# Kernel tuning notes

Hardware: AMD Instinct MI355X
Metric: run time of the kernel (lower is better)

Reference implementation:

```python
import jax, jax.numpy as jnp
import numpy as np

H = 12       # heads
D = 768      # hidden size
DH = D // H  # head dim = 64
SCALE = 1.0 / jnp.sqrt(jnp.float32(DH))
LN_EPS = 1e-3  # keras LayerNormalization default epsilon


def setup_inputs() -> dict:
    key = jax.random.key(0)
    ks = jax.random.split(key, 8)
    B, L = 16, 512
    s = 0.02  # truncated-normal-ish init scale
    return {
        "x": jax.random.normal(ks[0], (B, L, D), jnp.float32),
        "mask": jnp.ones((B, L), jnp.int32),
        "Wq": jax.random.normal(ks[1], (D, D), jnp.float32) * s,
        "bq": jnp.zeros((D,), jnp.float32),
        "Wk": jax.random.normal(ks[2], (D, D), jnp.float32) * s,
        "bk": jnp.zeros((D,), jnp.float32),
        "Wv": jax.random.normal(ks[3], (D, D), jnp.float32) * s,
        "bv": jnp.zeros((D,), jnp.float32),
        "Wo": jax.random.normal(ks[4], (D, D), jnp.float32) * s,
        "bo": jnp.zeros((D,), jnp.float32),
        "gamma": jnp.ones((D,), jnp.float32),
        "beta": jnp.zeros((D,), jnp.float32),
    }


def reference(x, mask, Wq, bq, Wk, bk, Wv, bv, Wo, bo, gamma, beta):
    B, L, _ = x.shape
    # QKV projections, split into heads: [B, L, H, DH]
    q = (x @ Wq + bq).reshape(B, L, H, DH)
    k = (x @ Wk + bk).reshape(B, L, H, DH)
    v = (x @ Wv + bv).reshape(B, L, H, DH)
    # scaled dot-product scores: [B, H, Lq, Lk]
    scores = jnp.einsum('bqhd,bkhd->bhqk', q, k) * SCALE
    # key-side padding mask (mask==0 -> -inf)
    neg = jnp.float32(-1e9)
    scores = jnp.where(mask[:, None, None, :] > 0, scores, neg)
    p = jax.nn.softmax(scores, axis=-1)
    # dropout rate fixed to 0.0 -> identity
    ctx = jnp.einsum('bhqk,bkhd->bqhd', p, v).reshape(B, L, D)
    attn_out = ctx @ Wo + bo
    # residual + LayerNorm (keras default eps=1e-3)
    y = x + attn_out
    mu = jnp.mean(y, axis=-1, keepdims=True)
    var = jnp.mean(jnp.square(y - mu), axis=-1, keepdims=True)
    return gamma * (y - mu) * jax.lax.rsqrt(var + LN_EPS) + beta
```

## Files before the change

kernel.cpp:

```cpp
#include <hip/hip_runtime.h>
#include <math.h>

#define NH 12
#define DMODEL 768
#define DHEAD 64
#define BATCH 16
#define SEQ 512
#define NTOK (BATCH*SEQ)
#define ATTN_SCALE 0.125f
#define LN_EPS 1e-3f
#define PADP 72
#define NKT 12

typedef __attribute__((ext_vector_type(8))) short  bf16x8;
typedef __attribute__((ext_vector_type(4))) float  f32x4;

__device__ __forceinline__ unsigned short f2bf(float f) {
    unsigned int u = __float_as_uint(f);
    unsigned int r = (u + 0x7fffu + ((u >> 16) & 1u)) >> 16;
    return (unsigned short)r;
}

__device__ __forceinline__ void async_copy16(const void* g, void* l) {
    __builtin_amdgcn_global_load_lds((const __attribute__((address_space(1))) void*)g,
                                     (__attribute__((address_space(3))) void*)l,
                                     16, 0, 0);
}

#define SBAR() do { \
    __builtin_amdgcn_sched_barrier(0); \
    __builtin_amdgcn_s_barrier(); \
    __builtin_amdgcn_sched_barrier(0); \
} while (0)

#define VMW0() do { \
    __builtin_amdgcn_sched_barrier(0); \
    asm volatile("s_waitcnt vmcnt(0)" ::: "memory"); \
    __builtin_amdgcn_sched_barrier(0); \
} while (0)

__global__ __launch_bounds__(256) void prep_kernel(
    const float* __restrict__ x,
    const float* __restrict__ Wq, const float* __restrict__ Wk,
    const float* __restrict__ Wv, const float* __restrict__ Wo,
    unsigned short* __restrict__ xb,
    unsigned short* __restrict__ tq, unsigned short* __restrict__ tk,
    unsigned short* __restrict__ tv, unsigned short* __restrict__ to_)
{
    __shared__ float tile[32][33];
    const int bid = blockIdx.x;
    const int tid = threadIdx.x;

    if (bid < 6144) {
        int i = (bid * 256 + tid) * 4;
        const float4 v = *(const float4*)(x + i);
        unsigned long long pack =
              (unsigned long long)f2bf(v.x)
            | ((unsigned long long)f2bf(v.y) << 16)
            | ((unsigned long long)f2bf(v.z) << 32)
            | ((unsigned long long)f2bf(v.w) << 48);
        *(unsigned long long*)(xb + i) = pack;
        return;
    }

    const int t   = bid - 6144;
    const int zz  = t / 576;
    const int rem = t % 576;
    const float* W = (zz == 0) ? Wq : (zz == 1) ? Wk : (zz == 2) ? Wv : Wo;
    unsigned short* T = (zz == 0) ? tq : (zz == 1) ? tk : (zz == 2) ? tv : to_;

    const int bx = (rem / 24) * 32;
    const int by = (rem % 24) * 32;
    const int tx = tid & 31, ty = tid >> 5;

    #pragma unroll
    for (int i = 0; i < 32; i += 8)
        tile[ty + i][tx] = W[(size_t)(bx + ty + i) * DMODEL + by + tx];
    __syncthreads();
    #pragma unroll
    for (int i = 0; i < 32; i += 8)
        T[(size_t)(by + ty + i) * DMODEL + bx + tx] = f2bf(tile[tx][ty + i]);
}

#define QSTAGE(kt, sb) do { \
    const int _k0 = (kt) * 64; \
    _Pragma("unroll") \
    for (int _i = 0; _i < 4; ++_i) \
        async_copy16(aSrc + (size_t)_i * (8 * DMODEL) + _k0, &As[sb][(w * 4 + _i) * 512]); \
    _Pragma("unroll") \
    for (int _i = 0; _i < 4; ++_i) \
        async_copy16(bSrc + (size_t)_i * (64 * DMODEL) + _k0, &Bs[sb][(w + 8 * _i) * 512]); \
    if (w < 4) \
        async_copy16(bSrc + (size_t)4 * (64 * DMODEL) + _k0, &Bs[sb][(w + 32) * 512]); \
} while (0)

#define QTILE(t, c, o, hasNext) do { \
    if (hasNext) QSTAGE((t) + 1, o); \
    bf16x8 aF[4][2]; \
    _Pragma("unroll") \
    for (int _m = 0; _m < 4; ++_m) { \
        const int _row = wm * 64 + _m * 16 + l16; \
        aF[_m][0] = *(const bf16x8*)&As[c][_row * 64 + p0]; \
        aF[_m][1] = *(const bf16x8*)&As[c][_row * 64 + (p0 ^ 32)]; \
    } \
    _Pragma("unroll") \
    for (int _nh = 0; _nh < 3; ++_nh) { \
        bf16x8 bF[3][2]; \
        _Pragma("unroll") \
        for (int _n = 0; _n < 3; ++_n) { \
            const int _row = wn * 144 + (_nh * 3 + _n) * 16 + l16; \
            bF[_n][0] = *(const bf16x8*)&Bs[c][_row * 64 + p0]; \
            bF[_n][1] = *(const bf16x8*)&Bs[c][_row * 64 + (p0 ^ 32)]; \
        } \
        __builtin_amdgcn_s_setprio(1); \
        _Pragma("unroll") \
        for (int _k = 0; _k < 2; ++_k) \
          _Pragma("unroll") \
          for (int _m = 0; _m < 4; ++_m) \
            _Pragma("unroll") \
            for (int _n = 0; _n < 3; ++_n) \
              acc[_m][_nh * 3 + _n] = __builtin_amdgcn_mfma_f32_16x16x32_bf16( \
                  aF[_m][_k], bF[_n][_k], acc[_m][_nh * 3 + _n], 0, 0, 0); \
        __builtin_amdgcn_s_setprio(0); \
    } \
    if (hasNext) VMW0(); \
    SBAR(); \
} while (0)

__global__ __launch_bounds__(512, 2) void gemm_db_qkv(
    const unsigned short* __restrict__ xb, const unsigned short* __restrict__ wt,
    const float* __restrict__ bq, const float* __restrict__ bk, const float* __restrict__ bv,
    unsigned short* __restrict__ o0, unsigned short* __restrict__ o1,
    unsigned short* __restrict__ o2)
{
    __shared__ __align__(16) unsigned short As[2][256 * 64];
    __shared__ __align__(16) unsigned short Bs[2][288 * 64];

    const int orig = blockIdx.x;
    const int wg   = (orig & 7) * 32 + (orig >> 3);
    const int m0   = (wg >> 3) * 256;
    const int n0   = (wg & 7) * 288;

    const int tid  = threadIdx.x;
    const int lane = tid & 63;
    const int w    = tid >> 6;
    const int wm   = w >> 1, wn = w & 1;
    const int quad = lane >> 4;
    const int l16  = lane & 15;
    const int rloc = lane >> 3;
    const int csw  = (lane & 7) ^ rloc;
    const int p0   = (quad ^ (l16 & 7)) * 8;

    const unsigned short* aSrc = xb + (size_t)(m0 + w * 32 + rloc) * DMODEL + csw * 8;
    const unsigned short* bSrc = wt + (size_t)(n0 + w * 8  + rloc) * DMODEL + csw * 8;

    f32x4 acc[4][9] = {};

    QSTAGE(0, 0);
    VMW0();
    SBAR();

    #pragma unroll 1
    for (int tt = 0; tt < NKT / 2; ++tt) {
        QTILE(2 * tt,     0, 1, 1);
        QTILE(2 * tt + 1, 1, 0, (tt < NKT / 2 - 1));
    }

    #pragma unroll
    for (int nf = 0; nf < 9; ++nf) {
        const int ncg = n0 + wn * 144 + nf * 16 + l16;
        const int zz  = (ncg >= 1536) ? 2 : (ncg >= 768) ? 1 : 0;
        const int ncl = ncg - zz * 768;
        const int h = ncl >> 6, dh = ncl & 63;
        const float bval = ((zz == 0) ? bq : (zz == 1) ? bk : bv)[ncl];
        if (zz == 2) {
            #pragma unroll
            for (int mi = 0; mi < 4; ++mi) {
                const int mbase = m0 + wm * 64 + mi * 16 + quad * 4;
                const int bi = mbase >> 9, l = mbase & 511;
                unsigned long long pack = 0;
                #pragma unroll
                for (int r = 0; r < 4; ++r)
                    pack |= (unsigned long long)f2bf(acc[mi][nf][r] + bval) << (16 * r);
                *(unsigned long long*)(o2 + ((size_t)((bi * NH + h) * DHEAD + dh)) * SEQ + l) = pack;
            }
        } else {
            const float sc = (zz == 0) ? ATTN_SCALE : 1.0f;
            unsigned short* out = (zz == 0) ? o0 : o1;
            #pragma unroll
            for (int mi = 0; mi < 4; ++mi) {
                const int mbase = m0 + wm * 64 + mi * 16 + quad * 4;
                #pragma unroll
                for (int r = 0; r < 4; ++r) {
                    const int t = mbase + r;
                    const int bi = t >> 9, l = t & 511;
                    out[(size_t)((bi * NH + h) * SEQ + l) * DHEAD + dh] =
                        f2bf((acc[mi][nf][r] + bval) * sc);
                }
            }
        }
    }
}

#define OSTAGE(kt, sb) do { \
    const int _k0 = (kt) * 64; \
    _Pragma("unroll") \
    for (int _i = 0; _i < 2; ++_i) \
        async_copy16(aSrc + (size_t)_i * (8 * DMODEL) + _k0, &Ao[sb][(w * 2 + _i) * 512]); \
    _Pragma("unroll") \
    for (int _i = 0; _i < 3; ++_i) \
        async_copy16(bSrc + (size_t)_i * (8 * DMODEL) + _k0, &Bo[sb][(w * 3 + _i) * 512]); \
} while (0)

#define OTILE(t, c, o, hasNext) do { \
    if (hasNext) OSTAGE((t) + 1, o); \
    bf16x8 aF[4][2], bF[3][2]; \
    _Pragma("unroll") \
    for (int _m = 0; _m < 4; ++_m) { \
        const int _row = wm * 64 + _m * 16 + l16; \
        aF[_m][0] = *(const bf16x8*)&Ao[c][_row * 64 + p0]; \
        aF[_m][1] = *(const bf16x8*)&Ao[c][_row * 64 + (p0 ^ 32)]; \
    } \
    _Pragma("unroll") \
    for (int _n = 0; _n < 3; ++_n) { \
        const int _row = wn * 48 + _n * 16 + l16; \
        bF[_n][0] = *(const bf16x8*)&Bo[c][_row * 64 + p0]; \
        bF[_n][1] = *(const bf16x8*)&Bo[c][_row * 64 + (p0 ^ 32)]; \
    } \
    __builtin_amdgcn_s_setprio(1); \
    _Pragma("unroll") \
    for (int _k = 0; _k < 2; ++_k) \
      _Pragma("unroll") \
      for (int _m = 0; _m < 4; ++_m) \
        _Pragma("unroll") \
        for (int _n = 0; _n < 3; ++_n) \
          acc[_m][_n] = __builtin_amdgcn_mfma_f32_16x16x32_bf16( \
              aF[_m][_k], bF[_n][_k], acc[_m][_n], 0, 0, 0); \
    __builtin_amdgcn_s_setprio(0); \
    if (hasNext) VMW0(); \
    SBAR(); \
} while (0)

__global__ __launch_bounds__(512, 2) void gemm_db_oproj(
    const unsigned short* __restrict__ ctxb, const unsigned short* __restrict__ wto,
    const float* __restrict__ bo, const float* __restrict__ x,
    float* __restrict__ y)
{
    __shared__ __align__(16) unsigned short Ao[2][132 * 64];
    __shared__ __align__(16) unsigned short Bo[2][192 * 64];

    const int orig = blockIdx.x;
    const int wg   = (orig & 7) * 32 + (orig >> 3);
    const int m0   = (wg >> 2) * 128;
    const int n0   = (wg & 3) * 192;

    const int tid  = threadIdx.x;
    const int lane = tid & 63;
    const int w    = tid >> 6;
    const int wm   = w >> 2, wn = w & 3;
    const int quad = lane >> 4;
    const int l16  = lane & 15;
    const int rloc = lane >> 3;
    const int csw  = (lane & 7) ^ rloc;
    const int p0   = (quad ^ (l16 & 7)) * 8;

    const unsigned short* aSrc = ctxb + (size_t)(m0 + w * 16 + rloc) * DMODEL + csw * 8;
    const unsigned short* bSrc = wto  + (size_t)(n0 + w * 24 + rloc) * DMODEL + csw * 8;

    f32x4 acc[4][3] = {};

    OSTAGE(0, 0);
    VMW0();
    SBAR();

    #pragma unroll 1
    for (int tt = 0; tt < NKT / 2; ++tt) {
        OTILE(2 * tt,     0, 1, 1);
        OTILE(2 * tt + 1, 1, 0, (tt < NKT / 2 - 1));
    }

    #pragma unroll
    for (int ni = 0; ni < 3; ++ni) {
        const int ncol = n0 + wn * 48 + ni * 16 + l16;
        const float bv_ = bo[ncol];
        #pragma unroll
        for (int mi = 0; mi < 4; ++mi) {
            const int mbase = m0 + wm * 64 + mi * 16 + quad * 4;
            #pragma unroll
            for (int r = 0; r < 4; ++r) {
                const size_t idx = (size_t)(mbase + r) * DMODEL + ncol;
                y[idx] = acc[mi][ni][r] + bv_ + x[idx];
            }
        }
    }
}

__global__ __launch_bounds__(256) void attn_mfma_kernel(
    const unsigned short* __restrict__ q, const unsigned short* __restrict__ k,
    const unsigned short* __restrict__ vt, const int* __restrict__ mask,
    unsigned short* __restrict__ ctxb)
{
    __shared__ __align__(16) unsigned short Qs[64 * 64];
    __shared__ __align__(16) unsigned short Ks[2][64 * 64];
    __shared__ __align__(16) unsigned short Vs[2][64 * 64];
    __shared__ __align__(16) unsigned short Ps[64 * PADP];
    __shared__ float maskV[SEQ];
    __shared__ int   cleanS[8];

    const int tid  = threadIdx.x;
    const int lane = tid & 63;
    const int w    = tid >> 6;
    const int quad = lane >> 4;
    const int l16  = lane & 15;

    const int id = blockIdx.x;
    const int qt = id / (BATCH * NH);
    const int g  = id % (BATCH * NH);
    const int b  = g / NH, h = g % NH;
    const int q0 = qt * 64;

    const unsigned short* qp  = q  + ((size_t)(b * NH + h) * SEQ + q0) * DHEAD;
    const unsigned short* kp  = k  + (size_t)(b * NH + h) * SEQ * DHEAD;
    const unsigned short* vtp = vt + (size_t)(b * NH + h) * DHEAD * SEQ;

    const int rloc = lane >> 3;
    const int csw  = (lane & 7) ^ rloc;
    const int p0   = (quad ^ (l16 & 7)) * 8;

    #pragma unroll
    for (int ii = 0; ii < 2; ++ii) {
        const int inst = 2 * w + ii;
        async_copy16(qp  + (size_t)(inst * 8 + rloc) * DHEAD + csw * 8, Qs + inst * 512);
        async_copy16(kp  + (size_t)(inst * 8 + rloc) * DHEAD + csw * 8, &Ks[0][inst * 512]);
        async_copy16(vtp + (size_t)(inst * 8 + rloc) * SEQ + csw * 8,   &Vs[0][inst * 512]);
    }
    #pragma unroll
    for (int j = 0; j < 2; ++j) {
        const int idx = tid + 256 * j;
        const bool pm = mask[b * SEQ + idx] > 0;
        maskV[idx] = pm ? 0.f : -1e9f;
        const unsigned long long bb = __ballot(pm);
        if (lane == 0) cleanS[w + 4 * j] = (bb == ~0ull) ? 1 : 0;
    }
    __syncthreads();

    bf16x8 aQ[2];
    #pragma unroll
    for (int ks = 0; ks < 2; ++ks)
        aQ[ks] = *(const bf16x8*)&Qs[(w * 16 + l16) * 64 + (p0 ^ (ks * 32))];

    bf16x8 ones;
    #pragma unroll
    for (int j = 0; j < 8; ++j) ones[j] = (short)0x3F80;

    f32x4 o[4] = {};
    f32x4 lsum = {0.f, 0.f, 0.f, 0.f};
    const f32x4 zf = {0.f, 0.f, 0.f, 0.f};

    #pragma unroll
    for (int it = 0; it < 8; ++it) {
        const int cur = it & 1;
        if (it + 1 < 8) {
            const int kt1 = (it + 1) * 64;
            #pragma unroll
            for (int ii = 0; ii < 2; ++ii) {
                const int inst = 2 * w + ii;
                async_copy16(kp  + (size_t)(kt1 + inst * 8 + rloc) * DHEAD + csw * 8,
                             &Ks[1 - cur][inst * 512]);
                async_copy16(vtp + (size_t)(inst * 8 + rloc) * SEQ + kt1 + csw * 8,
                             &Vs[1 - cur][inst * 512]);
            }
        }
        const int kt = it * 64;

        f32x4 s[4];
        #pragma unroll
        for (int ni = 0; ni < 4; ++ni) {
            bf16x8 bK0 = *(const bf16x8*)&Ks[cur][(ni * 16 + l16) * 64 + p0];
            bf16x8 bK1 = *(const bf16x8*)&Ks[cur][(ni * 16 + l16) * 64 + (p0 ^ 32)];
            f32x4 t0 = __builtin_amdgcn_mfma_f32_16x16x32_bf16(aQ[0], bK0, zf, 0, 0, 0);
            s[ni] = __builtin_amdgcn_mfma_f32_16x16x32_bf16(aQ[1], bK1, t0, 0, 0, 0);
        }
        if (cleanS[it] == 0) {
            #pragma unroll
            for (int ni = 0; ni < 4; ++ni) {
                const float mk = maskV[kt + ni * 16 + l16];
                #pragma unroll
                for (int r = 0; r < 4; ++r) s[ni][r] += mk;
            }
        }

        #pragma unroll
        for (int ni = 0; ni < 4; ++ni)
            #pragma unroll
            for (int r = 0; r < 4; ++r)
                Ps[(w * 16 + quad * 4 + r) * PADP + ni * 16 + l16]
                    = (unsigned short)(__float_as_uint(__expf(s[ni][r])) >> 16);

        bf16x8 aP[2];
        #pragma unroll
        for (int ks = 0; ks < 2; ++ks)
            aP[ks] = *(const bf16x8*)&Ps[(w * 16 + l16) * PADP + quad * 8 + ks * 32];

        lsum = __builtin_amdgcn_mfma_f32_16x16x32_bf16(aP[0], ones, lsum, 0, 0, 0);
        lsum = __builtin_amdgcn_mfma_f32_16x16x32_bf16(aP[1], ones, lsum, 0, 0, 0);

        #pragma unroll
        for (int ni = 0; ni < 4; ++ni) {
            bf16x8 bV0 = *(const bf16x8*)&Vs[cur][(ni * 16 + l16) * 64 + p0];
            bf16x8 bV1 = *(const bf16x8*)&Vs[cur][(ni * 16 + l16) * 64 + (p0 ^ 32)];
            o[ni] = __builtin_amdgcn_mfma_f32_16x16x32_bf16(aP[0], bV0, o[ni], 0, 0, 0);
            o[ni] = __builtin_amdgcn_mfma_f32_16x16x32_bf16(aP[1], bV1, o[ni], 0, 0, 0);
        }

        __syncthreads();
    }

    #pragma unroll
    for (int r = 0; r < 4; ++r) {
        const float inv = 1.f / lsum[r];
        const int tok = q0 + w * 16 + quad * 4 + r;
        #pragma unroll
        for (int ni = 0; ni < 4; ++ni)
            ctxb[(size_t)(b * SEQ + tok) * DMODEL + h * DHEAD + ni * 16 + l16]
                = f2bf(o[ni][r] * inv);
    }
}

__global__ __launch_bounds__(256) void ln_kernel(
    const float* __restrict__ y, const float* __restrict__ gamma,
    const float* __restrict__ beta, float* __restrict__ out)
{
    const int t   = blockIdx.x;
    const int tid = threadIdx.x;
    const float* row = y + (size_t)t * DMODEL;

    float vals[3];
    float s = 0.f, s2 = 0.f;
    #pragma unroll
    for (int i = 0; i < 3; ++i) {
        float vv = row[tid + 256 * i];
        vals[i] = vv;
        s  += vv;
        s2 += vv * vv;
    }
    #pragma unroll
    for (int off = 32; off > 0; off >>= 1) {
        s  += __shfl_down(s,  off);
        s2 += __shfl_down(s2, off);
    }
    __shared__ float rbuf[8];
    int w = tid >> 6;
    if ((tid & 63) == 0) { rbuf[w] = s; rbuf[4 + w] = s2; }
    __syncthreads();
    float ts  = rbuf[0] + rbuf[1] + rbuf[2] + rbuf[3];
    float ts2 = rbuf[4] + rbuf[5] + rbuf[6] + rbuf[7];
    float mu  = ts * (1.f / DMODEL);
    float var = ts2 * (1.f / DMODEL) - mu * mu;
    float inv = rsqrtf(var + LN_EPS);
    #pragma unroll
    for (int i = 0; i < 3; ++i) {
        int c = tid + 256 * i;
        out[(size_t)t * DMODEL + c] = gamma[c] * (vals[i] - mu) * inv + beta[c];
    }
}

extern "C" void kernel_launch(void* const* d_in, const int* in_sizes, int n_in,
                              void* d_out, int out_size, void* d_ws, size_t ws_size,
                              hipStream_t stream) {
    const float* x     = (const float*)d_in[0];
    const int*   mask  = (const int*)  d_in[1];
    const float* Wq    = (const float*)d_in[2];
    const float* bq    = (const float*)d_in[3];
    const float* Wk    = (const float*)d_in[4];
    const float* bk    = (const float*)d_in[5];
    const float* Wv    = (const float*)d_in[6];
    const float* bv    = (const float*)d_in[7];
    const float* Wo    = (const float*)d_in[8];
    const float* bo    = (const float*)d_in[9];
    const float* gamma = (const float*)d_in[10];
    const float* beta  = (const float*)d_in[11];
    float* out = (float*)d_out;

    const size_t perTok = (size_t)NTOK * DMODEL;
    const size_t perW   = (size_t)DMODEL * DMODEL;

    unsigned short* xb   = (unsigned short*)d_ws;
    unsigned short* wtq  = xb + perTok;
    unsigned short* wtk  = wtq + perW;
    unsigned short* wtv  = wtk + perW;
    unsigned short* wto  = wtv + perW;
    unsigned short* qb   = wto + perW;
    unsigned short* kb   = qb + perTok;
    unsigned short* vb   = kb + perTok;
    unsigned short* ctxb = vb + perTok;
    float* y = out;

    prep_kernel<<<6144 + 2304, 256, 0, stream>>>(
        x, Wq, Wk, Wv, Wo, xb, wtq, wtk, wtv, wto);

    gemm_db_qkv<<<256, 512, 0, stream>>>(xb, wtq, bq, bk, bv, qb, kb, vb);

    attn_mfma_kernel<<<dim3((SEQ / 64) * BATCH * NH), 256, 0, stream>>>(
        qb, kb, vb, mask, ctxb);

    gemm_db_oproj<<<256, 512, 0, stream>>>(ctxb, wto, bo, x, y);

    ln_kernel<<<NTOK, 256, 0, stream>>>(y, gamma, beta, out);
}
```

Baseline: 194.4 us.

## Process two query tiles per attention block to reuse K/V tiles

Each attention block now handles 128 query rows (two 64-row tiles) instead of 64, so each K/V tile loaded into shared memory feeds twice as many MFMAs and the grid is halved. Q fragments are loaded straight from global memory into registers rather than staged through LDS. The mask is now always added, with the exp folded in, replacing the per-tile clean-mask check. A launch-bounds occupancy hint is added. This roughly doubles accumulator registers and halves the number of blocks (768), which may reduce latency hiding and lowers the block count relative to the CU count.

```diff
diff --git a/kernel.cpp b/kernel.cpp
--- a/kernel.cpp
+++ b/kernel.cpp
@@ -295,17 +295,15 @@
     }
 }
 
-__global__ __launch_bounds__(256) void attn_mfma_kernel(
+__global__ __launch_bounds__(256, 3) void attn_mfma_kernel(
     const unsigned short* __restrict__ q, const unsigned short* __restrict__ k,
     const unsigned short* __restrict__ vt, const int* __restrict__ mask,
     unsigned short* __restrict__ ctxb)
 {
-    __shared__ __align__(16) unsigned short Qs[64 * 64];
     __shared__ __align__(16) unsigned short Ks[2][64 * 64];
     __shared__ __align__(16) unsigned short Vs[2][64 * 64];
-    __shared__ __align__(16) unsigned short Ps[64 * PADP];
+    __shared__ __align__(16) unsigned short Ps[2][64 * PADP];
     __shared__ float maskV[SEQ];
-    __shared__ int   cleanS[8];
 
     const int tid  = threadIdx.x;
     const int lane = tid & 63;
@@ -317,7 +315,7 @@
     const int qt = id / (BATCH * NH);
     const int g  = id % (BATCH * NH);
     const int b  = g / NH, h = g % NH;
-    const int q0 = qt * 64;
+    const int q0 = qt * 128;
 
     const unsigned short* qp  = q  + ((size_t)(b * NH + h) * SEQ + q0) * DHEAD;
     const unsigned short* kp  = k  + (size_t)(b * NH + h) * SEQ * DHEAD;
@@ -330,32 +328,32 @@
     #pragma unroll
     for (int ii = 0; ii < 2; ++ii) {
         const int inst = 2 * w + ii;
-        async_copy16(qp  + (size_t)(inst * 8 + rloc) * DHEAD + csw * 8, Qs + inst * 512);
         async_copy16(kp  + (size_t)(inst * 8 + rloc) * DHEAD + csw * 8, &Ks[0][inst * 512]);
         async_copy16(vtp + (size_t)(inst * 8 + rloc) * SEQ + csw * 8,   &Vs[0][inst * 512]);
     }
     #pragma unroll
     for (int j = 0; j < 2; ++j) {
         const int idx = tid + 256 * j;
-        const bool pm = mask[b * SEQ + idx] > 0;
-        maskV[idx] = pm ? 0.f : -1e9f;
-        const unsigned long long bb = __ballot(pm);
-        if (lane == 0) cleanS[w + 4 * j] = (bb == ~0ull) ? 1 : 0;
-    }
+        maskV[idx] = (mask[b * SEQ + idx] > 0) ? 0.f : -1e9f;
+    }
+
+    bf16x8 aQ[2][2];
+    #pragma unroll
+    for (int qtl = 0; qtl < 2; ++qtl)
+        #pragma unroll
+        for (int ks = 0; ks < 2; ++ks)
+            aQ[qtl][ks] = *(const bf16x8*)(qp + (size_t)(qtl * 64 + w * 16 + l16) * DHEAD
+                                              + ks * 32 + quad * 8);
+
+    bf16x8 ones;
+    #pragma unroll
+    for (int j = 0; j < 8; ++j) ones[j] = (short)0x3F80;
+
+    f32x4 o[2][4] = {};
+    f32x4 lsum[2] = {};
+    const f32x4 zf = {0.f, 0.f, 0.f, 0.f};
+
     __syncthreads();
-
-    bf16x8 aQ[2];
-    #pragma unroll
-    for (int ks = 0; ks < 2; ++ks)
-        aQ[ks] = *(const bf16x8*)&Qs[(w * 16 + l16) * 64 + (p0 ^ (ks * 32))];
-
-    bf16x8 ones;
-    #pragma unroll
-    for (int j = 0; j < 8; ++j) ones[j] = (short)0x3F80;
-
-    f32x4 o[4] = {};
-    f32x4 lsum = {0.f, 0.f, 0.f, 0.f};
-    const f32x4 zf = {0.f, 0.f, 0.f, 0.f};
 
     #pragma unroll
     for (int it = 0; it < 8; ++it) {
@@ -373,58 +371,64 @@
         }
         const int kt = it * 64;
 
-        f32x4 s[4];
+        f32x4 s[2][4];
         #pragma unroll
         for (int ni = 0; ni < 4; ++ni) {
             bf16x8 bK0 = *(const bf16x8*)&Ks[cur][(ni * 16 + l16) * 64 + p0];
             bf16x8 bK1 = *(const bf16x8*)&Ks[cur][(ni * 16 + l16) * 64 + (p0 ^ 32)];
-            f32x4 t0 = __builtin_amdgcn_mfma_f32_16x16x32_bf16(aQ[0], bK0, zf, 0, 0, 0);
-            s[ni] = __builtin_amdgcn_mfma_f32_16x16x32_bf16(aQ[1], bK1, t0, 0, 0, 0);
-        }
-        if (cleanS[it] == 0) {
-            #pragma unroll
-            for (int ni = 0; ni < 4; ++ni) {
-                const float mk = maskV[kt + ni * 16 + l16];
+            #pragma unroll
+            for (int qtl = 0; qtl < 2; ++qtl) {
+                f32x4 t0 = __builtin_amdgcn_mfma_f32_16x16x32_bf16(aQ[qtl][0], bK0, zf, 0, 0, 0);
+                s[qtl][ni] = __builtin_amdgcn_mfma_f32_16x16x32_bf16(aQ[qtl][1], bK1, t0, 0, 0, 0);
+            }
+        }
+
+        #pragma unroll
+        for (int ni = 0; ni < 4; ++ni) {
+            const float mk = maskV[kt + ni * 16 + l16];
+            #pragma unroll
+            for (int qtl = 0; qtl < 2; ++qtl)
                 #pragma unroll
-                for (int r = 0; r < 4; ++r) s[ni][r] += mk;
-            }
-        }
-
-        #pragma unroll
-        for (int ni = 0; ni < 4; ++ni)
-            #pragma unroll
-            for (int r = 0; r < 4; ++r)
-                Ps[(w * 16 + quad * 4 + r) * PADP + ni * 16 + l16]
-                    = (unsigned short)(__float_as_uint(__expf(s[ni][r])) >> 16);
-
-        bf16x8 aP[2];
-        #pragma unroll
-        for (int ks = 0; ks < 2; ++ks)
-            aP[ks] = *(const bf16x8*)&Ps[(w * 16 + l16) * PADP + quad * 8 + ks * 32];
-
-        lsum = __builtin_amdgcn_mfma_f32_16x16x32_bf16(aP[0], ones, lsum, 0, 0, 0);
-        lsum = __builtin_amdgcn_mfma_f32_16x16x32_bf16(aP[1], ones, lsum, 0, 0, 0);
+                for (int r = 0; r < 4; ++r)
+                    Ps[qtl][(w * 16 + quad * 4 + r) * PADP + ni * 16 + l16]
+                        = (unsigned short)(__float_as_uint(__expf(s[qtl][ni][r] + mk)) >> 16);
+        }
+
+        bf16x8 aP[2][2];
+        #pragma unroll
+        for (int qtl = 0; qtl < 2; ++qtl) {
+            #pragma unroll
+            for (int ks = 0; ks < 2; ++ks)
+                aP[qtl][ks] = *(const bf16x8*)&Ps[qtl][(w * 16 + l16) * PADP + quad * 8 + ks * 32];
+            lsum[qtl] = __builtin_amdgcn_mfma_f32_16x16x32_bf16(aP[qtl][0], ones, lsum[qtl], 0, 0, 0);
+            lsum[qtl] = __builtin_amdgcn_mfma_f32_16x16x32_bf16(aP[qtl][1], ones, lsum[qtl], 0, 0, 0);
+        }
 
         #pragma unroll
         for (int ni = 0; ni < 4; ++ni) {
             bf16x8 bV0 = *(const bf16x8*)&Vs[cur][(ni * 16 + l16) * 64 + p0];
             bf16x8 bV1 = *(const bf16x8*)&Vs[cur][(ni * 16 + l16) * 64 + (p0 ^ 32)];
-            o[ni] = __builtin_amdgcn_mfma_f32_16x16x32_bf16(aP[0], bV0, o[ni], 0, 0, 0);
-            o[ni] = __builtin_amdgcn_mfma_f32_16x16x32_bf16(aP[1], bV1, o[ni], 0, 0, 0);
+            #pragma unroll
+            for (int qtl = 0; qtl < 2; ++qtl) {
+                o[qtl][ni] = __builtin_amdgcn_mfma_f32_16x16x32_bf16(aP[qtl][0], bV0, o[qtl][ni], 0, 0, 0);
+                o[qtl][ni] = __builtin_amdgcn_mfma_f32_16x16x32_bf16(aP[qtl][1], bV1, o[qtl][ni], 0, 0, 0);
+            }
         }
 
         __syncthreads();
     }
 
     #pragma unroll
-    for (int r = 0; r < 4; ++r) {
-        const float inv = 1.f / lsum[r];
-        const int tok = q0 + w * 16 + quad * 4 + r;
-        #pragma unroll
-        for (int ni = 0; ni < 4; ++ni)
-            ctxb[(size_t)(b * SEQ + tok) * DMODEL + h * DHEAD + ni * 16 + l16]
-                = f2bf(o[ni][r] * inv);
-    }
+    for (int qtl = 0; qtl < 2; ++qtl)
+        #pragma unroll
+        for (int r = 0; r < 4; ++r) {
+            const float inv = 1.f / lsum[qtl][r];
+            const int tok = q0 + qtl * 64 + w * 16 + quad * 4 + r;
+            #pragma unroll
+            for (int ni = 0; ni < 4; ++ni)
+                ctxb[(size_t)(b * SEQ + tok) * DMODEL + h * DHEAD + ni * 16 + l16]
+                    = f2bf(o[qtl][ni][r] * inv);
+        }
 }
 
 __global__ __launch_bounds__(256) void ln_kernel(
@@ -501,7 +505,7 @@
 
     gemm_db_qkv<<<256, 512, 0, stream>>>(xb, wtq, bq, bk, bv, qb, kb, vb);
 
-    attn_mfma_kernel<<<dim3((SEQ / 64) * BATCH * NH), 256, 0, stream>>>(
+    attn_mfma_kernel<<<dim3((SEQ / 128) * BATCH * NH), 256, 0, stream>>>(
         qb, kb, vb, mask, ctxb);
 
     gemm_db_oproj<<<256, 512, 0, stream>>>(ctxb, wto, bo, x, y);
```

New measurement: 188.2 us. 1.03x faster.
